# Kernel tuning notes

Hardware: AMD Instinct MI355X
Metric: run time of the kernel (lower is better)

The kernel has to match this reference:

```python
import jax, jax.numpy as jnp
import numpy as np

BN_EPS = 1e-5


def setup_inputs() -> dict:
    key = jax.random.key(0)
    ks = jax.random.split(key, 12)
    B, N, S, D1, D2 = 2, 16384, 4096, 128, 256
    C1, C2 = 256, 128  # mlp channels
    return {
        "xyz1": jax.random.normal(ks[0], (B, 3, N), dtype=jnp.float32),
        "xyz2": jax.random.normal(ks[1], (B, 3, S), dtype=jnp.float32),
        "points1": jax.random.normal(ks[2], (B, D1, N), dtype=jnp.float32),
        "points2": jax.random.normal(ks[3], (B, D2, S), dtype=jnp.float32),
        "w1": jax.random.normal(ks[4], (D1 + D2, C1), dtype=jnp.float32) * 0.05,
        "b1": jax.random.normal(ks[5], (C1,), dtype=jnp.float32) * 0.05,
        "g1": jax.random.uniform(ks[6], (C1,), dtype=jnp.float32, minval=0.5, maxval=1.5),
        "beta1": jax.random.normal(ks[7], (C1,), dtype=jnp.float32) * 0.05,
        "w2": jax.random.normal(ks[8], (C1, C2), dtype=jnp.float32) * 0.05,
        "b2": jax.random.normal(ks[9], (C2,), dtype=jnp.float32) * 0.05,
        "g2": jax.random.uniform(ks[10], (C2,), dtype=jnp.float32, minval=0.5, maxval=1.5),
        "beta2": jax.random.normal(ks[11], (C2,), dtype=jnp.float32) * 0.05,
    }


def _conv_bn_relu(x, W, b, g, beta):
    # 1x1 Conv1d == per-point matmul; BatchNorm1d training-mode stats over (B, N).
    y = x @ W + b                              # [B, N, Cout]
    mu = jnp.mean(y, axis=(0, 1))
    var = jnp.var(y, axis=(0, 1))              # biased variance, matches torch BN
    y = g * (y - mu) * jax.lax.rsqrt(var + BN_EPS) + beta
    return jax.nn.relu(y)


def reference(xyz1, xyz2, points1, points2, w1, b1, g1, beta1, w2, b2, g2, beta2):
    x1 = jnp.transpose(xyz1, (0, 2, 1))        # [B, N, 3]
    x2 = jnp.transpose(xyz2, (0, 2, 1))        # [B, S, 3]
    p2 = jnp.transpose(points2, (0, 2, 1))     # [B, S, D2]

    # squared pairwise distance [B, N, S], clamped at 0
    d = (jnp.sum(x1 ** 2, axis=-1, keepdims=True)
         - 2.0 * jnp.einsum('bnc,bsc->bns', x1, x2)
         + jnp.sum(x2 ** 2, axis=-1)[:, None, :])
    d = jnp.maximum(d, 0.0)

    # 3 nearest neighbors (ascending smallest distances) -- same math as full sort + slice
    neg_d3, idx = jax.lax.top_k(-d, 3)         # [B, N, 3]
    d3 = jnp.maximum(-neg_d3, 1e-6)
    recip = 1.0 / d3
    w = recip / jnp.maximum(jnp.sum(recip, axis=-1, keepdims=True), 1e-6)

    nb = jax.vmap(lambda p, i: p[i])(p2, idx)  # [B, N, 3, D2]
    interp = jnp.sum(nb * w[..., None], axis=2)
    interp = jnp.nan_to_num(interp, nan=0.0, posinf=0.0, neginf=0.0)

    p1 = jnp.transpose(points1, (0, 2, 1))     # [B, N, D1]
    x = jnp.concatenate([p1, interp], axis=-1) # [B, N, D1+D2]

    x = _conv_bn_relu(x, w1, b1, g1, beta1)
    x = _conv_bn_relu(x, w2, b2, g2, beta2)
    x = jnp.nan_to_num(x, nan=0.0, posinf=0.0, neginf=0.0)
    return jnp.transpose(x, (0, 2, 1))         # [B, C2, N]
```

## Files before the change

kernel.cpp:

```cpp
#include <hip/hip_runtime.h>

#define B_   2
#define N_   16384
#define S_   4096
#define D1_  128
#define D2_  256
#define C1_  256
#define C2_  128
#define M_   (B_ * N_)

typedef __bf16 bf16_t;
typedef bf16_t bf16x8 __attribute__((ext_vector_type(8)));
typedef float  f32x4  __attribute__((ext_vector_type(4)));

__device__ __forceinline__ void gload16(const void* g, void* l) {
  __builtin_amdgcn_global_load_lds(
      (const __attribute__((address_space(1))) void*)g,
      (__attribute__((address_space(3))) void*)l, 16, 0, 0);
}

__device__ __forceinline__ float med3a(float a, float b, float c) {
  float d;
  asm("v_med3_f32 %0, %1, %2, %3" : "=v"(d) : "v"(a), "v"(b), "v"(c));
  return d;
}

__device__ __forceinline__ float4 cand4(const float* __restrict__ X2, int i) {
  float x = X2[i], y = X2[S_ + i], z = X2[2 * S_ + i];
  float w = fmaf(x, x, fmaf(y, y, z * z));
  return make_float4(-2.f * x, -2.f * y, -2.f * z, w);
}
__device__ __forceinline__ float distv(float4 c, float ax, float ay, float az) {
  return fmaf(ax, c.x, fmaf(ay, c.y, fmaf(az, c.z, c.w)));
}
#define TRACK3(v)                                                        \
  {                                                                      \
    float t0_ = fminf((v), m0);                                          \
    float t1_ = med3a((v), m0, m1);                                      \
    float t2_ = med3a((v), m1, m2);                                      \
    m0 = t0_; m1 = t1_; m2 = t2_;                                        \
  }

union SMem1 {
  struct { float4 cbuf[1024]; float T3V[2][3][32]; float QMv[32][3]; } knn;
  float tile[2][32][33];
};

__global__ __launch_bounds__(512, 8) void phase1_k(const float* __restrict__ xyz1,
                                                   const float* __restrict__ xyz2,
                                                   const float* __restrict__ points1,
                                                   const float* __restrict__ w1,
                                                   const float* __restrict__ w2,
                                                   float* __restrict__ kw,
                                                   int* __restrict__ ki,
                                                   bf16_t* __restrict__ Xp1,
                                                   bf16_t* __restrict__ w1at,
                                                   bf16_t* __restrict__ w2t) {
  __shared__ SMem1 sm;
  int bi = blockIdx.x, t = threadIdx.x;
  if (bi < 1024) {
    int l = t & 63, w = t >> 6;
    int q = l & 31, h = l >> 5;
    int s = w * 2 + h;
    int b  = bi >> 9;
    int nb = (bi & 511) * 32;
    int n  = nb + q;
    const float* X1 = xyz1 + (size_t)b * 3 * N_;
    const float* X2 = xyz2 + (size_t)b * 3 * S_;
    float ax = X1[n], ay = X1[N_ + n], az = X1[2 * N_ + n];
    float p = fmaf(ax, ax, fmaf(ay, ay, az * az));
    float m0 = 3e38f, m1 = 3e38f, m2 = 3e38f;
    for (int r = 0; r < 4; ++r) {
      __syncthreads();
      sm.knn.cbuf[t]       = cand4(X2, r * 1024 + t);
      sm.knn.cbuf[t + 512] = cand4(X2, r * 1024 + t + 512);
      __syncthreads();
      const float4* cs = sm.knn.cbuf + s * 64;
#pragma unroll 16
      for (int i = 0; i < 64; ++i) {
        float v = distv(cs[i], ax, ay, az);
        TRACK3(v);
      }
    }
    __syncthreads();
    float* SV = (float*)sm.knn.cbuf;
    SV[(s * 3 + 0) * 32 + q] = m0;  SV[(s * 3 + 1) * 32 + q] = m1;  SV[(s * 3 + 2) * 32 + q] = m2;
    __syncthreads();
    if (t < 64) {
      int th = t >> 5, tq = t & 31;
      float m0 = 3e38f, m1 = 3e38f, m2 = 3e38f;
      for (int s2 = th * 8; s2 < th * 8 + 8; ++s2)
#pragma unroll
        for (int k = 0; k < 3; ++k) {
          float v = SV[(s2 * 3 + k) * 32 + tq];
          TRACK3(v);
        }
      sm.knn.T3V[th][0][tq] = m0; sm.knn.T3V[th][1][tq] = m1; sm.knn.T3V[th][2][tq] = m2;
    }
    __syncthreads();
    float g0 = 3e38f, g1 = 3e38f, g2 = 3e38f;
    if (t < 32) {
      float m0 = sm.knn.T3V[0][0][t], m1 = sm.knn.T3V[0][1][t], m2 = sm.knn.T3V[0][2][t];
#pragma unroll
      for (int k = 0; k < 3; ++k) {
        float v = sm.knn.T3V[1][k][t];
        TRACK3(v);
      }
      g0 = m0; g1 = m1; g2 = m2;
      sm.knn.QMv[t][0] = m0; sm.knn.QMv[t][1] = m1; sm.knn.QMv[t][2] = m2;
    }
    __syncthreads();
    float q0v = sm.knn.QMv[q][0], q1v = sm.knn.QMv[q][1], q2v = sm.knn.QMv[q][2];
    unsigned j0 = 0xFFFFFFFFu, j1 = 0xFFFFFFFFu, j2 = 0xFFFFFFFFu;
    for (int r = 0; r < 4; ++r) {
      __syncthreads();
      sm.knn.cbuf[t]       = cand4(X2, r * 1024 + t);
      sm.knn.cbuf[t + 512] = cand4(X2, r * 1024 + t + 512);
      __syncthreads();
      const float4* cs = sm.knn.cbuf + s * 64;
      int base = r * 1024 + s * 64;
#pragma unroll
      for (int g = 0; g < 16; ++g) {
        float v0 = distv(cs[g * 4 + 0], ax, ay, az);
        float v1 = distv(cs[g * 4 + 1], ax, ay, az);
        float v2 = distv(cs[g * 4 + 2], ax, ay, az);
        float v3 = distv(cs[g * 4 + 3], ax, ay, az);
        float gm = fminf(fminf(v0, v1), fminf(v2, v3));
        if (gm <= q2v) {
#define CHK(vv, uu)                                                      \
          {                                                              \
            unsigned idx = (unsigned)(base + g * 4 + uu);                \
            bool h0 = ((vv) == q0v) && (j0 == 0xFFFFFFFFu);              \
            bool h1 = ((vv) == q1v) && (j1 == 0xFFFFFFFFu) && !h0;       \
            bool h2 = ((vv) == q2v) && (j2 == 0xFFFFFFFFu) && !h0 && !h1;\
            if (h0) j0 = idx;                                            \
            if (h1) j1 = idx;                                            \
            if (h2) j2 = idx;                                            \
          }
          CHK(v0, 0) CHK(v1, 1) CHK(v2, 2) CHK(v3, 3)
#undef CHK
        }
      }
    }
    __syncthreads();
    unsigned* SI = (unsigned*)sm.knn.cbuf;
    SI[(s * 3 + 0) * 32 + q] = j0;  SI[(s * 3 + 1) * 32 + q] = j1;  SI[(s * 3 + 2) * 32 + q] = j2;
    __syncthreads();
    if (t < 32) {
      unsigned a0 = 0xFFFFFFFFu, a1 = 0xFFFFFFFFu, a2 = 0xFFFFFFFFu;
      for (int s2 = 0; s2 < 16; ++s2) {
        a0 = min(a0, SI[(s2 * 3 + 0) * 32 + t]);
        a1 = min(a1, SI[(s2 * 3 + 1) * 32 + t]);
        a2 = min(a2, SI[(s2 * 3 + 2) * 32 + t]);
      }
      a0 = min(a0, (unsigned)(S_ - 1));
      a1 = min(a1, (unsigned)(S_ - 1));
      a2 = min(a2, (unsigned)(S_ - 1));
      float d0 = fmaxf(p + g0, 1e-6f);
      float d1 = fmaxf(p + g1, 1e-6f);
      float d2 = fmaxf(p + g2, 1e-6f);
      float r0 = 1.f / d0, r1 = 1.f / d1, r2 = 1.f / d2;
      float dn = fmaxf(r0 + r1 + r2, 1e-6f);
      size_t rr = (size_t)b * N_ + n;
      kw[rr * 3 + 0] = r0 / dn;  kw[rr * 3 + 1] = r1 / dn;  kw[rr * 3 + 2] = r2 / dn;
      ki[rr * 3 + 0] = (int)a0;  ki[rr * 3 + 1] = (int)a1;  ki[rr * 3 + 2] = (int)a2;
    }
  } else if (bi < 3072) {
    int bj = bi - 1024;
    int b = bj >> 10, rest = bj & 1023;
    int n0 = (rest & 255) * 64, c0 = (rest >> 8) * 32;
    int tx = t & 31, ty = (t >> 5) & 7, th = t >> 8;
    const float* src = points1 + (size_t)b * D1_ * N_;
#pragma unroll
    for (int k = 0; k < 4; ++k)
      sm.tile[th][ty + k * 8][tx] = src[(size_t)(c0 + ty + k * 8) * N_ + n0 + th * 32 + tx];
    __syncthreads();
#pragma unroll
    for (int k = 0; k < 4; ++k)
      Xp1[(size_t)(b * N_ + n0 + th * 32 + ty + k * 8) * 128 + c0 + tx] =
          (bf16_t)sm.tile[th][tx][ty + k * 8];
  } else {
    int i = (bi - 3072) * 512 + t;
    if (i < 32768) {
      int n = i >> 7, k = i & 127;
      w1at[i] = (bf16_t)w1[(size_t)k * C1_ + n];
    } else {
      int j = i - 32768;
      int n = j >> 8, k = j & 255;
      w2t[j] = (bf16_t)w2[(size_t)k * C2_ + n];
    }
  }
}

__global__ __launch_bounds__(512) void gemmG_k(const float* __restrict__ points2,
                                               const float* __restrict__ w1,
                                               bf16_t* __restrict__ G) {
  const int LDP = 40;
  __shared__ bf16_t As[128 * LDP];
  __shared__ bf16_t Bs[256 * LDP];
  int t = threadIdx.x, lane = t & 63, w = t >> 6;
  int wr = w >> 2, wc = w & 3;
  int bb = blockIdx.x >> 5;
  int m0 = (blockIdx.x & 31) * 128;
  const float* P2 = points2 + (size_t)bb * D2_ * S_;
  f32x4 acc[4][4];
  f32x4 z = {0.f, 0.f, 0.f, 0.f};
#pragma unroll
  for (int i = 0; i < 4; ++i)
#pragma unroll
    for (int j = 0; j < 4; ++j) acc[i][j] = z;
  int sA = t & 127, kgA = t >> 7;
  int nB = t & 255, kgB = t >> 8;
  for (int k0 = 0; k0 < 256; k0 += 32) {
    __syncthreads();
    {
      bf16x8 ap;
#pragma unroll
      for (int kk = 0; kk < 8; ++kk)
        ap[kk] = (bf16_t)P2[(size_t)(k0 + kgA * 8 + kk) * S_ + m0 + sA];
      *(bf16x8*)&As[sA * LDP + kgA * 8] = ap;
      bf16x8 bp0, bp1;
#pragma unroll
      for (int kk = 0; kk < 8; ++kk) {
        bp0[kk] = (bf16_t)w1[(size_t)(128 + k0 + kgB * 16 + kk) * C1_ + nB];
        bp1[kk] = (bf16_t)w1[(size_t)(128 + k0 + kgB * 16 + 8 + kk) * C1_ + nB];
      }
      *(bf16x8*)&Bs[nB * LDP + kgB * 16] = bp0;
      *(bf16x8*)&Bs[nB * LDP + kgB * 16 + 8] = bp1;
    }
    __syncthreads();
    bf16x8 af[4], bfr[4];
    int arow = wr * 64 + (lane & 15);
    int brow = wc * 64 + (lane & 15);
    int kc = 8 * (lane >> 4);
#pragma unroll
    for (int i = 0; i < 4; ++i) af[i]  = *(const bf16x8*)&As[(arow + i * 16) * LDP + kc];
#pragma unroll
    for (int j = 0; j < 4; ++j) bfr[j] = *(const bf16x8*)&Bs[(brow + j * 16) * LDP + kc];
#pragma unroll
    for (int i = 0; i < 4; ++i)
#pragma unroll
      for (int j = 0; j < 4; ++j)
        acc[i][j] = __builtin_amdgcn_mfma_f32_16x16x32_bf16(af[i], bfr[j], acc[i][j], 0, 0, 0);
  }
  bf16_t* Gb = G + (size_t)bb * S_ * 256;
#pragma unroll
  for (int j = 0; j < 4; ++j) {
    int col = wc * 64 + j * 16 + (lane & 15);
#pragma unroll
    for (int i = 0; i < 4; ++i) {
      int r = m0 + wr * 64 + i * 16 + ((lane >> 4) << 2);
#pragma unroll
      for (int q = 0; q < 4; ++q)
        Gb[(size_t)(r + q) * 256 + col] = (bf16_t)acc[i][j][q];
    }
  }
}

__global__ __launch_bounds__(512) void gemm1_k(const bf16_t* __restrict__ A,
                                               const bf16_t* __restrict__ Bt,
                                               const float* __restrict__ bias,
                                               const bf16_t* __restrict__ G,
                                               const float* __restrict__ KW,
                                               const int* __restrict__ KI,
                                               bf16_t* __restrict__ Y,
                                               float* __restrict__ st) {
  const int K = 128;
  __shared__ bf16_t As[128 * 32];
  __shared__ bf16_t Bs[256 * 32];
  int tid = threadIdx.x, lane = tid & 63, w = tid >> 6;
  int wr = w >> 2, wc = w & 3;
  int m0 = blockIdx.x * 128;
  int ra = tid >> 2, ca = (tid & 3) * 8;
  f32x4 acc[4][4];
  f32x4 z = {0.f, 0.f, 0.f, 0.f};
#pragma unroll
  for (int i = 0; i < 4; ++i)
#pragma unroll
    for (int j = 0; j < 4; ++j) acc[i][j] = z;
  for (int k0 = 0; k0 < K; k0 += 32) {
    __syncthreads();
    gload16(A + (size_t)(m0 + ra) * K + k0 + ca, &As[ra * 32 + ca]);
    gload16(Bt + (size_t)ra * K + k0 + ca, &Bs[ra * 32 + ca]);
    gload16(Bt + (size_t)(128 + ra) * K + k0 + ca, &Bs[(128 + ra) * 32 + ca]);
    __syncthreads();
    bf16x8 af[4], bfr[4];
    int arow = wr * 64 + (lane & 15);
    int brow = wc * 64 + (lane & 15);
    int kc = 8 * (lane >> 4);
#pragma unroll
    for (int i = 0; i < 4; ++i) af[i]  = *(const bf16x8*)&As[(arow + i * 16) * 32 + kc];
#pragma unroll
    for (int j = 0; j < 4; ++j) bfr[j] = *(const bf16x8*)&Bs[(brow + j * 16) * 32 + kc];
#pragma unroll
    for (int i = 0; i < 4; ++i)
#pragma unroll
      for (int j = 0; j < 4; ++j)
        acc[i][j] = __builtin_amdgcn_mfma_f32_16x16x32_bf16(af[i], bfr[j], acc[i][j], 0, 0, 0);
  }
  __syncthreads();
  float* kwls = (float*)As;
  int*   kils = ((int*)As) + 384;
  if (tid < 128) {
    int r = m0 + tid;
    kwls[tid * 3 + 0] = KW[(size_t)r * 3 + 0];
    kwls[tid * 3 + 1] = KW[(size_t)r * 3 + 1];
    kwls[tid * 3 + 2] = KW[(size_t)r * 3 + 2];
    kils[tid * 3 + 0] = KI[(size_t)r * 3 + 0];
    kils[tid * 3 + 1] = KI[(size_t)r * 3 + 1];
    kils[tid * 3 + 2] = KI[(size_t)r * 3 + 2];
  }
  __syncthreads();
  int bb = m0 >> 14;
  const bf16_t* Gb = G + (size_t)bb * S_ * 256;
  float sjv[4]  = {0.f, 0.f, 0.f, 0.f};
  float ssjv[4] = {0.f, 0.f, 0.f, 0.f};
#pragma unroll
  for (int i = 0; i < 4; ++i) {
#pragma unroll
    for (int qq = 0; qq < 4; ++qq) {
      int rl = wr * 64 + i * 16 + ((lane >> 4) << 2) + qq;
      float w0 = kwls[rl * 3 + 0], w1v = kwls[rl * 3 + 1], w2v = kwls[rl * 3 + 2];
      const bf16_t* g0 = Gb + (size_t)kils[rl * 3 + 0] * 256;
      const bf16_t* g1 = Gb + (size_t)kils[rl * 3 + 1] * 256;
      const bf16_t* g2 = Gb + (size_t)kils[rl * 3 + 2] * 256;
      int r = m0 + rl;
#pragma unroll
      for (int j = 0; j < 4; ++j) {
        int col = wc * 64 + j * 16 + (lane & 15);
        float y = acc[i][j][qq] + bias[col]
                + w0 * (float)g0[col] + w1v * (float)g1[col] + w2v * (float)g2[col];
        Y[(size_t)r * C1_ + col] = (bf16_t)y;
        sjv[j] += y;  ssjv[j] += y * y;
      }
    }
  }
#pragma unroll
  for (int j = 0; j < 4; ++j) {
    float sj = sjv[j], ssj = ssjv[j];
    sj  += __shfl_xor(sj, 16);  sj  += __shfl_xor(sj, 32);
    ssj += __shfl_xor(ssj, 16); ssj += __shfl_xor(ssj, 32);
    if ((lane >> 4) == 0) {
      int col = wc * 64 + j * 16 + (lane & 15);
      atomicAdd(&st[col], sj);
      atomicAdd(&st[C1_ + col], ssj);
    }
  }
}

__global__ __launch_bounds__(256) void gemm2_k(const bf16_t* __restrict__ Y1,
                                               const bf16_t* __restrict__ Bt,
                                               const float* __restrict__ bias,
                                               const float* __restrict__ st1,
                                               const float* __restrict__ g1v,
                                               const float* __restrict__ be1,
                                               float* __restrict__ OUT,
                                               float* __restrict__ st2) {
  const int K = 256;
  __shared__ bf16_t As[128 * 32];
  __shared__ bf16_t Bs[128 * 32];
  __shared__ float sa1[C1_], sb1[C1_];
  int tid = threadIdx.x, lane = tid & 63, w = tid >> 6;
  int wr = w >> 1, wc = w & 1;
  int m0 = blockIdx.x * 128;
  {
    const float invM = 1.f / (float)M_;
    float mu  = st1[tid] * invM;
    float var = fmaxf(st1[C1_ + tid] * invM - mu * mu, 0.f);
    float a = g1v[tid] * rsqrtf(var + 1e-5f);
    sa1[tid] = a;
    sb1[tid] = be1[tid] - mu * a;
  }
  int e0 = (w * 2 + 0) * 512 + lane * 8;
  int e1 = (w * 2 + 1) * 512 + lane * 8;
  int ra0 = e0 >> 5, ca0 = e0 & 31;
  int ra1 = e1 >> 5, ca1 = e1 & 31;
  f32x4 acc[4][4];
  f32x4 z = {0.f, 0.f, 0.f, 0.f};
#pragma unroll
  for (int i = 0; i < 4; ++i)
#pragma unroll
    for (int j = 0; j < 4; ++j) acc[i][j] = z;
  bf16x8 va0 = *(const bf16x8*)&Y1[(size_t)(m0 + ra0) * C1_ + ca0];
  bf16x8 va1 = *(const bf16x8*)&Y1[(size_t)(m0 + ra1) * C1_ + ca1];
  __syncthreads();
  for (int k0 = 0; k0 < K; k0 += 32) {
    bf16x8 nb0, nb1;
    if (k0 + 32 < K) {
      nb0 = *(const bf16x8*)&Y1[(size_t)(m0 + ra0) * C1_ + k0 + 32 + ca0];
      nb1 = *(const bf16x8*)&Y1[(size_t)(m0 + ra1) * C1_ + k0 + 32 + ca1];
    }
    if (k0) __syncthreads();
    bf16x8 oa0, oa1;
#pragma unroll
    for (int u = 0; u < 8; ++u) {
      float f0 = (float)va0[u];
      float f1 = (float)va1[u];
      f0 = fmaxf(f0 * sa1[k0 + ca0 + u] + sb1[k0 + ca0 + u], 0.f);
      f1 = fmaxf(f1 * sa1[k0 + ca1 + u] + sb1[k0 + ca1 + u], 0.f);
      oa0[u] = (bf16_t)f0;
      oa1[u] = (bf16_t)f1;
    }
    *(bf16x8*)&As[e0] = oa0;
    *(bf16x8*)&As[e1] = oa1;
    gload16(Bt + (size_t)ra0 * K + k0 + ca0, &Bs[e0]);
    gload16(Bt + (size_t)ra1 * K + k0 + ca1, &Bs[e1]);
    __syncthreads();
    bf16x8 af[4], bfr[4];
    int arow = wr * 64 + (lane & 15);
    int brow = wc * 64 + (lane & 15);
    int kc = 8 * (lane >> 4);
#pragma unroll
    for (int i = 0; i < 4; ++i) af[i]  = *(const bf16x8*)&As[(arow + i * 16) * 32 + kc];
#pragma unroll
    for (int j = 0; j < 4; ++j) bfr[j] = *(const bf16x8*)&Bs[(brow + j * 16) * 32 + kc];
#pragma unroll
    for (int i = 0; i < 4; ++i)
#pragma unroll
      for (int j = 0; j < 4; ++j)
        acc[i][j] = __builtin_amdgcn_mfma_f32_16x16x32_bf16(af[i], bfr[j], acc[i][j], 0, 0, 0);
    va0 = nb0; va1 = nb1;
  }
#pragma unroll
  for (int j = 0; j < 4; ++j) {
    int col = wc * 64 + j * 16 + (lane & 15);
    float bv = bias[col];
    float sj = 0.f, ssj = 0.f;
#pragma unroll
    for (int i = 0; i < 4; ++i) {
      int r  = m0 + wr * 64 + i * 16 + ((lane >> 4) << 2);
      int bb = r >> 14, n = r & (N_ - 1);
      f32x4 v = acc[i][j];
#pragma unroll
      for (int q = 0; q < 4; ++q) {
        v[q] += bv;
        sj += v[q]; ssj += v[q] * v[q];
      }
      *(f32x4*)&OUT[((size_t)(bb * C2_ + col)) * N_ + n] = v;
    }
    sj  += __shfl_xor(sj, 16);  sj  += __shfl_xor(sj, 32);
    ssj += __shfl_xor(ssj, 16); ssj += __shfl_xor(ssj, 32);
    if ((lane >> 4) == 0) {
      atomicAdd(&st2[col], sj);
      atomicAdd(&st2[C2_ + col], ssj);
    }
  }
}

__global__ __launch_bounds__(256) void bn2apply_k(float* __restrict__ OUT,
                                                  const float* __restrict__ st,
                                                  const float* __restrict__ g,
                                                  const float* __restrict__ be) {
  __shared__ float ab[2];
  int t = threadIdx.x;
  int c = (blockIdx.x >> 4) & 127;
  if (t == 0) {
    const float invM = 1.f / (float)M_;
    float mu  = st[c] * invM;
    float var = fmaxf(st[C2_ + c] * invM - mu * mu, 0.f);
    float a = g[c] * rsqrtf(var + 1e-5f);
    ab[0] = a;
    ab[1] = be[c] - mu * a;
  }
  __syncthreads();
  float a = ab[0], s = ab[1];
  size_t i4 = (size_t)blockIdx.x * 256 + t;
  f32x4 v = *(f32x4*)&OUT[i4 * 4];
#pragma unroll
  for (int u = 0; u < 4; ++u) v[u] = fmaxf(a * v[u] + s, 0.f);
  *(f32x4*)&OUT[i4 * 4] = v;
}

extern "C" void kernel_launch(void* const* d_in, const int* in_sizes, int n_in,
                              void* d_out, int out_size, void* d_ws, size_t ws_size,
                              hipStream_t stream) {
  const float* xyz1    = (const float*)d_in[0];
  const float* xyz2    = (const float*)d_in[1];
  const float* points1 = (const float*)d_in[2];
  const float* points2 = (const float*)d_in[3];
  const float* w1      = (const float*)d_in[4];
  const float* b1      = (const float*)d_in[5];
  const float* g1      = (const float*)d_in[6];
  const float* beta1   = (const float*)d_in[7];
  const float* w2      = (const float*)d_in[8];
  const float* b2      = (const float*)d_in[9];
  const float* g2      = (const float*)d_in[10];
  const float* beta2   = (const float*)d_in[11];
  float* out = (float*)d_out;

  char* p = (char*)d_ws;
  size_t off = 0;
  bf16_t* Xp1  = (bf16_t*)(p + off); off += (size_t)M_ * 128 * 2;
  bf16_t* W1AT = (bf16_t*)(p + off); off += (size_t)C1_ * 128 * 2;
  bf16_t* W2T  = (bf16_t*)(p + off); off += (size_t)C2_ * C1_ * 2;
  bf16_t* G    = (bf16_t*)(p + off); off += (size_t)B_ * S_ * 256 * 2;
  bf16_t* Y1   = (bf16_t*)(p + off); off += (size_t)M_ * C1_ * 2;
  float*  KW   = (float*)(p + off);  off += (size_t)M_ * 3 * 4;
  int*    KI   = (int*)(p + off);    off += (size_t)M_ * 3 * 4;
  float*  ST1  = (float*)(p + off);  off += 2048;
  float*  ST2  = (float*)(p + off);  off += 1024;

  hipMemsetAsync(ST1, 0, 3072, stream);

  phase1_k<<<3200, 512, 0, stream>>>(xyz1, xyz2, points1, w1, w2,
                                     KW, KI, Xp1, W1AT, W2T);
  gemmG_k<<<64, 512, 0, stream>>>(points2, w1, G);
  gemm1_k<<<M_ / 128, 512, 0, stream>>>(Xp1, W1AT, b1, G, KW, KI, Y1, ST1);
  gemm2_k<<<M_ / 128, 256, 0, stream>>>(Y1, W2T, b2, ST1, g1, beta1, out, ST2);
  bn2apply_k<<<4096, 256, 0, stream>>>(out, ST2, g2, beta2);
}
```

Baseline: 130.0 us.

## Fold G GEMM into phase1 and fuse BN2 apply into gemm2 via grid barrier

The standalone points2×W1b GEMM moves into the phase1 launch as 128 extra blocks, each computing a 128×128 tile so it fits the shared-memory union. The stats zeroing moves into phase1, replacing the separate memset. The final BN2+ReLU pass becomes the tail of gemm2: a global atomic counter barrier waits for all blocks' statistics, then each block normalizes its own output tile. This removes two kernel launches and a memset, and reuses the output while it may still be cached. It relies on all 256 gemm2 blocks being co-resident; if they are not, the spin barrier deadlocks.

```diff
diff --git a/kernel.cpp b/kernel.cpp
--- a/kernel.cpp
+++ b/kernel.cpp
@@ -41,21 +41,27 @@
     m0 = t0_; m1 = t1_; m2 = t2_;                                        \
   }
 
+#define LDPG 40
+
 union SMem1 {
   struct { float4 cbuf[1024]; float T3V[2][3][32]; float QMv[32][3]; } knn;
+  struct { bf16_t As[128 * LDPG]; bf16_t Bs[128 * LDPG]; } gg;
   float tile[2][32][33];
 };
 
 __global__ __launch_bounds__(512, 8) void phase1_k(const float* __restrict__ xyz1,
                                                    const float* __restrict__ xyz2,
                                                    const float* __restrict__ points1,
+                                                   const float* __restrict__ points2,
                                                    const float* __restrict__ w1,
                                                    const float* __restrict__ w2,
                                                    float* __restrict__ kw,
                                                    int* __restrict__ ki,
                                                    bf16_t* __restrict__ Xp1,
                                                    bf16_t* __restrict__ w1at,
-                                                   bf16_t* __restrict__ w2t) {
+                                                   bf16_t* __restrict__ w2t,
+                                                   bf16_t* __restrict__ G,
+                                                   float* __restrict__ stz) {
   __shared__ SMem1 sm;
   int bi = blockIdx.x, t = threadIdx.x;
   if (bi < 1024) {
@@ -179,7 +185,10 @@
     for (int k = 0; k < 4; ++k)
       Xp1[(size_t)(b * N_ + n0 + th * 32 + ty + k * 8) * 128 + c0 + tx] =
           (bf16_t)sm.tile[th][tx][ty + k * 8];
-  } else {
+  } else if (bi < 3200) {
+    if (bi == 3072) {
+      for (int z = t; z < 772; z += 512) stz[z] = 0.f;
+    }
     int i = (bi - 3072) * 512 + t;
     if (i < 32768) {
       int n = i >> 7, k = i & 127;
@@ -189,70 +198,56 @@
       int n = j >> 8, k = j & 255;
       w2t[j] = (bf16_t)w2[(size_t)k * C2_ + n];
     }
-  }
-}
-
-__global__ __launch_bounds__(512) void gemmG_k(const float* __restrict__ points2,
-                                               const float* __restrict__ w1,
-                                               bf16_t* __restrict__ G) {
-  const int LDP = 40;
-  __shared__ bf16_t As[128 * LDP];
-  __shared__ bf16_t Bs[256 * LDP];
-  int t = threadIdx.x, lane = t & 63, w = t >> 6;
-  int wr = w >> 2, wc = w & 3;
-  int bb = blockIdx.x >> 5;
-  int m0 = (blockIdx.x & 31) * 128;
-  const float* P2 = points2 + (size_t)bb * D2_ * S_;
-  f32x4 acc[4][4];
-  f32x4 z = {0.f, 0.f, 0.f, 0.f};
-#pragma unroll
-  for (int i = 0; i < 4; ++i)
-#pragma unroll
-    for (int j = 0; j < 4; ++j) acc[i][j] = z;
-  int sA = t & 127, kgA = t >> 7;
-  int nB = t & 255, kgB = t >> 8;
-  for (int k0 = 0; k0 < 256; k0 += 32) {
-    __syncthreads();
-    {
-      bf16x8 ap;
-#pragma unroll
-      for (int kk = 0; kk < 8; ++kk)
-        ap[kk] = (bf16_t)P2[(size_t)(k0 + kgA * 8 + kk) * S_ + m0 + sA];
-      *(bf16x8*)&As[sA * LDP + kgA * 8] = ap;
-      bf16x8 bp0, bp1;
-#pragma unroll
-      for (int kk = 0; kk < 8; ++kk) {
-        bp0[kk] = (bf16_t)w1[(size_t)(128 + k0 + kgB * 16 + kk) * C1_ + nB];
-        bp1[kk] = (bf16_t)w1[(size_t)(128 + k0 + kgB * 16 + 8 + kk) * C1_ + nB];
-      }
-      *(bf16x8*)&Bs[nB * LDP + kgB * 16] = bp0;
-      *(bf16x8*)&Bs[nB * LDP + kgB * 16 + 8] = bp1;
-    }
-    __syncthreads();
-    bf16x8 af[4], bfr[4];
-    int arow = wr * 64 + (lane & 15);
-    int brow = wc * 64 + (lane & 15);
-    int kc = 8 * (lane >> 4);
-#pragma unroll
-    for (int i = 0; i < 4; ++i) af[i]  = *(const bf16x8*)&As[(arow + i * 16) * LDP + kc];
-#pragma unroll
-    for (int j = 0; j < 4; ++j) bfr[j] = *(const bf16x8*)&Bs[(brow + j * 16) * LDP + kc];
-#pragma unroll
-    for (int i = 0; i < 4; ++i)
-#pragma unroll
-      for (int j = 0; j < 4; ++j)
-        acc[i][j] = __builtin_amdgcn_mfma_f32_16x16x32_bf16(af[i], bfr[j], acc[i][j], 0, 0, 0);
-  }
-  bf16_t* Gb = G + (size_t)bb * S_ * 256;
-#pragma unroll
-  for (int j = 0; j < 4; ++j) {
-    int col = wc * 64 + j * 16 + (lane & 15);
-#pragma unroll
-    for (int i = 0; i < 4; ++i) {
-      int r = m0 + wr * 64 + i * 16 + ((lane >> 4) << 2);
-#pragma unroll
-      for (int q = 0; q < 4; ++q)
-        Gb[(size_t)(r + q) * 256 + col] = (bf16_t)acc[i][j][q];
+  } else {
+    int idx = bi - 3200;
+    int bb = idx >> 6, rem = idx & 63;
+    int m0 = (rem >> 1) * 128, n0 = (rem & 1) * 128;
+    const float* P2 = points2 + (size_t)bb * D2_ * S_;
+    int lane = t & 63, w = t >> 6;
+    int wr = w >> 2, wc = w & 3;
+    f32x4 acc[4][2];
+    f32x4 z = {0.f, 0.f, 0.f, 0.f};
+#pragma unroll
+    for (int i = 0; i < 4; ++i) { acc[i][0] = z; acc[i][1] = z; }
+    int sA = t & 127, kg = t >> 7;
+    for (int k0 = 0; k0 < 256; k0 += 32) {
+      __syncthreads();
+      {
+        bf16x8 ap, bp;
+#pragma unroll
+        for (int kk = 0; kk < 8; ++kk) {
+          ap[kk] = (bf16_t)P2[(size_t)(k0 + kg * 8 + kk) * S_ + m0 + sA];
+          bp[kk] = (bf16_t)w1[(size_t)(128 + k0 + kg * 8 + kk) * C1_ + n0 + sA];
+        }
+        *(bf16x8*)&sm.gg.As[sA * LDPG + kg * 8] = ap;
+        *(bf16x8*)&sm.gg.Bs[sA * LDPG + kg * 8] = bp;
+      }
+      __syncthreads();
+      int arow = wr * 64 + (lane & 15);
+      int brow = wc * 32 + (lane & 15);
+      int kc = 8 * (lane >> 4);
+      bf16x8 bfr[2];
+#pragma unroll
+      for (int j = 0; j < 2; ++j) bfr[j] = *(const bf16x8*)&sm.gg.Bs[(brow + j * 16) * LDPG + kc];
+#pragma unroll
+      for (int i = 0; i < 4; ++i) {
+        bf16x8 af = *(const bf16x8*)&sm.gg.As[(arow + i * 16) * LDPG + kc];
+#pragma unroll
+        for (int j = 0; j < 2; ++j)
+          acc[i][j] = __builtin_amdgcn_mfma_f32_16x16x32_bf16(af, bfr[j], acc[i][j], 0, 0, 0);
+      }
+    }
+    bf16_t* Gb = G + (size_t)bb * S_ * 256;
+#pragma unroll
+    for (int j = 0; j < 2; ++j) {
+      int col = n0 + wc * 32 + j * 16 + (lane & 15);
+#pragma unroll
+      for (int i = 0; i < 4; ++i) {
+        int r = m0 + wr * 64 + i * 16 + ((lane >> 4) << 2);
+#pragma unroll
+        for (int q = 0; q < 4; ++q)
+          Gb[(size_t)(r + q) * 256 + col] = (bf16_t)acc[i][j][q];
+      }
     }
   }
 }
@@ -355,7 +350,10 @@
                                                const float* __restrict__ g1v,
                                                const float* __restrict__ be1,
                                                float* __restrict__ OUT,
-                                               float* __restrict__ st2) {
+                                               float* __restrict__ st2,
+                                               const float* __restrict__ g2v,
+                                               const float* __restrict__ be2,
+                                               int* __restrict__ cnt) {
   const int K = 256;
   __shared__ bf16_t As[128 * 32];
   __shared__ bf16_t Bs[128 * 32];
@@ -445,30 +443,36 @@
       atomicAdd(&st2[C2_ + col], ssj);
     }
   }
-}
-
-__global__ __launch_bounds__(256) void bn2apply_k(float* __restrict__ OUT,
-                                                  const float* __restrict__ st,
-                                                  const float* __restrict__ g,
-                                                  const float* __restrict__ be) {
-  __shared__ float ab[2];
-  int t = threadIdx.x;
-  int c = (blockIdx.x >> 4) & 127;
-  if (t == 0) {
+  __syncthreads();
+  if (tid == 0) {
+    __threadfence();
+    atomicAdd(cnt, 1);
+    while (__hip_atomic_load(cnt, __ATOMIC_ACQUIRE, __HIP_MEMORY_SCOPE_AGENT) < (int)gridDim.x)
+      __builtin_amdgcn_s_sleep(8);
+  }
+  __syncthreads();
+  if (tid < C2_) {
+    float s  = __hip_atomic_load(&st2[tid],       __ATOMIC_RELAXED, __HIP_MEMORY_SCOPE_AGENT);
+    float ss = __hip_atomic_load(&st2[C2_ + tid], __ATOMIC_RELAXED, __HIP_MEMORY_SCOPE_AGENT);
     const float invM = 1.f / (float)M_;
-    float mu  = st[c] * invM;
-    float var = fmaxf(st[C2_ + c] * invM - mu * mu, 0.f);
-    float a = g[c] * rsqrtf(var + 1e-5f);
-    ab[0] = a;
-    ab[1] = be[c] - mu * a;
+    float mu  = s * invM;
+    float var = fmaxf(ss * invM - mu * mu, 0.f);
+    float a = g2v[tid] * rsqrtf(var + 1e-5f);
+    sa1[tid] = a;
+    sb1[tid] = be2[tid] - mu * a;
   }
   __syncthreads();
-  float a = ab[0], s = ab[1];
-  size_t i4 = (size_t)blockIdx.x * 256 + t;
-  f32x4 v = *(f32x4*)&OUT[i4 * 4];
-#pragma unroll
-  for (int u = 0; u < 4; ++u) v[u] = fmaxf(a * v[u] + s, 0.f);
-  *(f32x4*)&OUT[i4 * 4] = v;
+  int bb = m0 >> 14, ng = m0 & (N_ - 1);
+  int c = tid >> 1, half = tid & 1;
+  float a = sa1[c], sft = sb1[c];
+  float* pr = OUT + ((size_t)(bb * C2_ + c)) * N_ + ng + half * 64;
+#pragma unroll
+  for (int u2 = 0; u2 < 16; ++u2) {
+    f32x4 v = *(f32x4*)&pr[u2 * 4];
+#pragma unroll
+    for (int u = 0; u < 4; ++u) v[u] = fmaxf(a * v[u] + sft, 0.f);
+    *(f32x4*)&pr[u2 * 4] = v;
+  }
 }
 
 extern "C" void kernel_launch(void* const* d_in, const int* in_sizes, int n_in,
@@ -499,13 +503,12 @@
   int*    KI   = (int*)(p + off);    off += (size_t)M_ * 3 * 4;
   float*  ST1  = (float*)(p + off);  off += 2048;
   float*  ST2  = (float*)(p + off);  off += 1024;
-
-  hipMemsetAsync(ST1, 0, 3072, stream);
-
-  phase1_k<<<3200, 512, 0, stream>>>(xyz1, xyz2, points1, w1, w2,
-                                     KW, KI, Xp1, W1AT, W2T);
-  gemmG_k<<<64, 512, 0, stream>>>(points2, w1, G);
+  int*    CNT  = (int*)(p + off);    off += 16;
+
+
+  phase1_k<<<3328, 512, 0, stream>>>(xyz1, xyz2, points1, points2, w1, w2,
+                                     KW, KI, Xp1, W1AT, W2T, G, ST1);
   gemm1_k<<<M_ / 128, 512, 0, stream>>>(Xp1, W1AT, b1, G, KW, KI, Y1, ST1);
-  gemm2_k<<<M_ / 128, 256, 0, stream>>>(Y1, W2T, b2, ST1, g1, beta1, out, ST2);
-  bn2apply_k<<<4096, 256, 0, stream>>>(out, ST2, g2, beta2);
-}
+  gemm2_k<<<M_ / 128, 256, 0, stream>>>(Y1, W2T, b2, ST1, g1, beta1,
+                                        out, ST2, g2, beta2, CNT);
+}
```

Measured after the change: 138.3 us. 1.06x slower.

## Fuse both GEMMs and BN2 apply into one persistent kernel with grid barriers

Applied to the files above, without the earlier changes.

Merges gemm1, gemm2 and bn2apply into a single kernel launched with 256 blocks. Each block keeps its 128-row Y1 tile in LDS instead of writing it to global memory. Two atomic-counter grid barriers wait until the BN1 and BN2 statistics are complete, and then each block normalizes its own tile in place. The separate memset is dropped: the stats buffers and counters are zeroed inside phase1. This removes the Y1 global write and read and two kernel launches. In exchange it relies on every block being co-resident (about 94KB of LDS per block), runs at low occupancy, and pays for the spin-wait barriers.

```diff
diff --git a/kernel.cpp b/kernel.cpp
--- a/kernel.cpp
+++ b/kernel.cpp
@@ -55,7 +55,8 @@
                                                    int* __restrict__ ki,
                                                    bf16_t* __restrict__ Xp1,
                                                    bf16_t* __restrict__ w1at,
-                                                   bf16_t* __restrict__ w2t) {
+                                                   bf16_t* __restrict__ w2t,
+                                                   float* __restrict__ stz) {
   __shared__ SMem1 sm;
   int bi = blockIdx.x, t = threadIdx.x;
   if (bi < 1024) {
@@ -180,6 +181,9 @@
       Xp1[(size_t)(b * N_ + n0 + th * 32 + ty + k * 8) * 128 + c0 + tx] =
           (bf16_t)sm.tile[th][tx][ty + k * 8];
   } else {
+    if (bi == 3072) {
+      for (int z = t; z < 772; z += 512) stz[z] = 0.f;
+    }
     int i = (bi - 3072) * 512 + t;
     if (i < 32768) {
       int n = i >> 7, k = i & 127;
@@ -257,17 +261,28 @@
   }
 }
 
-__global__ __launch_bounds__(512) void gemm1_k(const bf16_t* __restrict__ A,
-                                               const bf16_t* __restrict__ Bt,
-                                               const float* __restrict__ bias,
-                                               const bf16_t* __restrict__ G,
-                                               const float* __restrict__ KW,
-                                               const int* __restrict__ KI,
-                                               bf16_t* __restrict__ Y,
-                                               float* __restrict__ st) {
-  const int K = 128;
+#define LDY 264
+
+__global__ __launch_bounds__(512) void gemm12_k(const bf16_t* __restrict__ A,
+                                                const bf16_t* __restrict__ W1t,
+                                                const float* __restrict__ b1v,
+                                                const bf16_t* __restrict__ G,
+                                                const float* __restrict__ KW,
+                                                const int* __restrict__ KI,
+                                                float* __restrict__ st1,
+                                                const float* __restrict__ g1v,
+                                                const float* __restrict__ be1,
+                                                const bf16_t* __restrict__ W2t,
+                                                const float* __restrict__ b2v,
+                                                float* __restrict__ OUT,
+                                                float* __restrict__ st2,
+                                                const float* __restrict__ g2v,
+                                                const float* __restrict__ be2,
+                                                int* __restrict__ cnt) {
   __shared__ bf16_t As[128 * 32];
   __shared__ bf16_t Bs[256 * 32];
+  __shared__ bf16_t Y1L[128 * LDY];
+  __shared__ float sc1[C1_], sc2[C1_];
   int tid = threadIdx.x, lane = tid & 63, w = tid >> 6;
   int wr = w >> 2, wc = w & 3;
   int m0 = blockIdx.x * 128;
@@ -278,11 +293,11 @@
   for (int i = 0; i < 4; ++i)
 #pragma unroll
     for (int j = 0; j < 4; ++j) acc[i][j] = z;
-  for (int k0 = 0; k0 < K; k0 += 32) {
-    __syncthreads();
-    gload16(A + (size_t)(m0 + ra) * K + k0 + ca, &As[ra * 32 + ca]);
-    gload16(Bt + (size_t)ra * K + k0 + ca, &Bs[ra * 32 + ca]);
-    gload16(Bt + (size_t)(128 + ra) * K + k0 + ca, &Bs[(128 + ra) * 32 + ca]);
+  for (int k0 = 0; k0 < 128; k0 += 32) {
+    __syncthreads();
+    gload16(A + (size_t)(m0 + ra) * 128 + k0 + ca, &As[ra * 32 + ca]);
+    gload16(W1t + (size_t)ra * 128 + k0 + ca, &Bs[ra * 32 + ca]);
+    gload16(W1t + (size_t)(128 + ra) * 128 + k0 + ca, &Bs[(128 + ra) * 32 + ca]);
     __syncthreads();
     bf16x8 af[4], bfr[4];
     int arow = wr * 64 + (lane & 15);
@@ -313,130 +328,111 @@
   __syncthreads();
   int bb = m0 >> 14;
   const bf16_t* Gb = G + (size_t)bb * S_ * 256;
-  float sjv[4]  = {0.f, 0.f, 0.f, 0.f};
-  float ssjv[4] = {0.f, 0.f, 0.f, 0.f};
-#pragma unroll
-  for (int i = 0; i < 4; ++i) {
-#pragma unroll
-    for (int qq = 0; qq < 4; ++qq) {
-      int rl = wr * 64 + i * 16 + ((lane >> 4) << 2) + qq;
-      float w0 = kwls[rl * 3 + 0], w1v = kwls[rl * 3 + 1], w2v = kwls[rl * 3 + 2];
-      const bf16_t* g0 = Gb + (size_t)kils[rl * 3 + 0] * 256;
-      const bf16_t* g1 = Gb + (size_t)kils[rl * 3 + 1] * 256;
-      const bf16_t* g2 = Gb + (size_t)kils[rl * 3 + 2] * 256;
-      int r = m0 + rl;
-#pragma unroll
-      for (int j = 0; j < 4; ++j) {
+  {
+    float sjv[4]  = {0.f, 0.f, 0.f, 0.f};
+    float ssjv[4] = {0.f, 0.f, 0.f, 0.f};
+#pragma unroll
+    for (int i = 0; i < 4; ++i) {
+#pragma unroll
+      for (int qq = 0; qq < 4; ++qq) {
+        int rl = wr * 64 + i * 16 + ((lane >> 4) << 2) + qq;
+        float w0 = kwls[rl * 3 + 0], w1v = kwls[rl * 3 + 1], w2v = kwls[rl * 3 + 2];
+        const bf16_t* g0 = Gb + (size_t)kils[rl * 3 + 0] * 256;
+        const bf16_t* g1 = Gb + (size_t)kils[rl * 3 + 1] * 256;
+        const bf16_t* g2 = Gb + (size_t)kils[rl * 3 + 2] * 256;
+#pragma unroll
+        for (int j = 0; j < 4; ++j) {
+          int col = wc * 64 + j * 16 + (lane & 15);
+          float y = acc[i][j][qq] + b1v[col]
+                  + w0 * (float)g0[col] + w1v * (float)g1[col] + w2v * (float)g2[col];
+          Y1L[rl * LDY + col] = (bf16_t)y;
+          sjv[j] += y;  ssjv[j] += y * y;
+        }
+      }
+    }
+#pragma unroll
+    for (int j = 0; j < 4; ++j) {
+      float sj = sjv[j], ssj = ssjv[j];
+      sj  += __shfl_xor(sj, 16);  sj  += __shfl_xor(sj, 32);
+      ssj += __shfl_xor(ssj, 16); ssj += __shfl_xor(ssj, 32);
+      if ((lane >> 4) == 0) {
         int col = wc * 64 + j * 16 + (lane & 15);
-        float y = acc[i][j][qq] + bias[col]
-                + w0 * (float)g0[col] + w1v * (float)g1[col] + w2v * (float)g2[col];
-        Y[(size_t)r * C1_ + col] = (bf16_t)y;
-        sjv[j] += y;  ssjv[j] += y * y;
-      }
-    }
-  }
-#pragma unroll
-  for (int j = 0; j < 4; ++j) {
-    float sj = sjv[j], ssj = ssjv[j];
-    sj  += __shfl_xor(sj, 16);  sj  += __shfl_xor(sj, 32);
-    ssj += __shfl_xor(ssj, 16); ssj += __shfl_xor(ssj, 32);
-    if ((lane >> 4) == 0) {
-      int col = wc * 64 + j * 16 + (lane & 15);
-      atomicAdd(&st[col], sj);
-      atomicAdd(&st[C1_ + col], ssj);
-    }
-  }
-}
-
-__global__ __launch_bounds__(256) void gemm2_k(const bf16_t* __restrict__ Y1,
-                                               const bf16_t* __restrict__ Bt,
-                                               const float* __restrict__ bias,
-                                               const float* __restrict__ st1,
-                                               const float* __restrict__ g1v,
-                                               const float* __restrict__ be1,
-                                               float* __restrict__ OUT,
-                                               float* __restrict__ st2) {
-  const int K = 256;
-  __shared__ bf16_t As[128 * 32];
-  __shared__ bf16_t Bs[128 * 32];
-  __shared__ float sa1[C1_], sb1[C1_];
-  int tid = threadIdx.x, lane = tid & 63, w = tid >> 6;
-  int wr = w >> 1, wc = w & 1;
-  int m0 = blockIdx.x * 128;
-  {
+        atomicAdd(&st1[col], sj);
+        atomicAdd(&st1[C1_ + col], ssj);
+      }
+    }
+  }
+  __syncthreads();
+  if (tid == 0) {
+    __threadfence();
+    atomicAdd(&cnt[0], 1);
+    while (__hip_atomic_load(&cnt[0], __ATOMIC_ACQUIRE, __HIP_MEMORY_SCOPE_AGENT) < (int)gridDim.x)
+      __builtin_amdgcn_s_sleep(8);
+  }
+  __syncthreads();
+  if (tid < C1_) {
+    float s  = __hip_atomic_load(&st1[tid],       __ATOMIC_RELAXED, __HIP_MEMORY_SCOPE_AGENT);
+    float ss = __hip_atomic_load(&st1[C1_ + tid], __ATOMIC_RELAXED, __HIP_MEMORY_SCOPE_AGENT);
     const float invM = 1.f / (float)M_;
-    float mu  = st1[tid] * invM;
-    float var = fmaxf(st1[C1_ + tid] * invM - mu * mu, 0.f);
+    float mu  = s * invM;
+    float var = fmaxf(ss * invM - mu * mu, 0.f);
     float a = g1v[tid] * rsqrtf(var + 1e-5f);
-    sa1[tid] = a;
-    sb1[tid] = be1[tid] - mu * a;
-  }
-  int e0 = (w * 2 + 0) * 512 + lane * 8;
-  int e1 = (w * 2 + 1) * 512 + lane * 8;
-  int ra0 = e0 >> 5, ca0 = e0 & 31;
-  int ra1 = e1 >> 5, ca1 = e1 & 31;
-  f32x4 acc[4][4];
-  f32x4 z = {0.f, 0.f, 0.f, 0.f};
-#pragma unroll
-  for (int i = 0; i < 4; ++i)
-#pragma unroll
-    for (int j = 0; j < 4; ++j) acc[i][j] = z;
-  bf16x8 va0 = *(const bf16x8*)&Y1[(size_t)(m0 + ra0) * C1_ + ca0];
-  bf16x8 va1 = *(const bf16x8*)&Y1[(size_t)(m0 + ra1) * C1_ + ca1];
-  __syncthreads();
-  for (int k0 = 0; k0 < K; k0 += 32) {
-    bf16x8 nb0, nb1;
-    if (k0 + 32 < K) {
-      nb0 = *(const bf16x8*)&Y1[(size_t)(m0 + ra0) * C1_ + k0 + 32 + ca0];
-      nb1 = *(const bf16x8*)&Y1[(size_t)(m0 + ra1) * C1_ + k0 + 32 + ca1];
-    }
-    if (k0) __syncthreads();
-    bf16x8 oa0, oa1;
-#pragma unroll
-    for (int u = 0; u < 8; ++u) {
-      float f0 = (float)va0[u];
-      float f1 = (float)va1[u];
-      f0 = fmaxf(f0 * sa1[k0 + ca0 + u] + sb1[k0 + ca0 + u], 0.f);
-      f1 = fmaxf(f1 * sa1[k0 + ca1 + u] + sb1[k0 + ca1 + u], 0.f);
-      oa0[u] = (bf16_t)f0;
-      oa1[u] = (bf16_t)f1;
-    }
-    *(bf16x8*)&As[e0] = oa0;
-    *(bf16x8*)&As[e1] = oa1;
-    gload16(Bt + (size_t)ra0 * K + k0 + ca0, &Bs[e0]);
-    gload16(Bt + (size_t)ra1 * K + k0 + ca1, &Bs[e1]);
-    __syncthreads();
-    bf16x8 af[4], bfr[4];
+    sc1[tid] = a;
+    sc2[tid] = be1[tid] - mu * a;
+  }
+  __syncthreads();
+#pragma unroll
+  for (int u = 0; u < 8; ++u) {
+    int chunk = tid * 8 + u;
+    int row = chunk >> 5, cc = (chunk & 31) * 8;
+    bf16x8 v = *(bf16x8*)&Y1L[row * LDY + cc];
+    bf16x8 o;
+#pragma unroll
+    for (int u2 = 0; u2 < 8; ++u2) {
+      float f = (float)v[u2];
+      f = fmaxf(f * sc1[cc + u2] + sc2[cc + u2], 0.f);
+      o[u2] = (bf16_t)f;
+    }
+    *(bf16x8*)&Y1L[row * LDY + cc] = o;
+  }
+  __syncthreads();
+  f32x4 acc2[4][2];
+#pragma unroll
+  for (int i = 0; i < 4; ++i) { acc2[i][0] = z; acc2[i][1] = z; }
+  for (int k0 = 0; k0 < 256; k0 += 32) {
+    __syncthreads();
+    gload16(W2t + (size_t)ra * 256 + k0 + ca, &Bs[ra * 32 + ca]);
+    __syncthreads();
+    bf16x8 af[4], bfr[2];
     int arow = wr * 64 + (lane & 15);
-    int brow = wc * 64 + (lane & 15);
+    int brow = wc * 32 + (lane & 15);
     int kc = 8 * (lane >> 4);
 #pragma unroll
-    for (int i = 0; i < 4; ++i) af[i]  = *(const bf16x8*)&As[(arow + i * 16) * 32 + kc];
-#pragma unroll
-    for (int j = 0; j < 4; ++j) bfr[j] = *(const bf16x8*)&Bs[(brow + j * 16) * 32 + kc];
+    for (int i = 0; i < 4; ++i) af[i]  = *(const bf16x8*)&Y1L[(arow + i * 16) * LDY + k0 + kc];
+#pragma unroll
+    for (int j = 0; j < 2; ++j) bfr[j] = *(const bf16x8*)&Bs[(brow + j * 16) * 32 + kc];
 #pragma unroll
     for (int i = 0; i < 4; ++i)
 #pragma unroll
-      for (int j = 0; j < 4; ++j)
-        acc[i][j] = __builtin_amdgcn_mfma_f32_16x16x32_bf16(af[i], bfr[j], acc[i][j], 0, 0, 0);
-    va0 = nb0; va1 = nb1;
-  }
-#pragma unroll
-  for (int j = 0; j < 4; ++j) {
-    int col = wc * 64 + j * 16 + (lane & 15);
-    float bv = bias[col];
+      for (int j = 0; j < 2; ++j)
+        acc2[i][j] = __builtin_amdgcn_mfma_f32_16x16x32_bf16(af[i], bfr[j], acc2[i][j], 0, 0, 0);
+  }
+  int ng = m0 & (N_ - 1);
+#pragma unroll
+  for (int j = 0; j < 2; ++j) {
+    int col = wc * 32 + j * 16 + (lane & 15);
+    float bv = b2v[col];
     float sj = 0.f, ssj = 0.f;
 #pragma unroll
     for (int i = 0; i < 4; ++i) {
-      int r  = m0 + wr * 64 + i * 16 + ((lane >> 4) << 2);
-      int bb = r >> 14, n = r & (N_ - 1);
-      f32x4 v = acc[i][j];
+      int rl = wr * 64 + i * 16 + ((lane >> 4) << 2);
+      f32x4 v = acc2[i][j];
 #pragma unroll
       for (int q = 0; q < 4; ++q) {
         v[q] += bv;
         sj += v[q]; ssj += v[q] * v[q];
       }
-      *(f32x4*)&OUT[((size_t)(bb * C2_ + col)) * N_ + n] = v;
+      *(f32x4*)&OUT[((size_t)(bb * C2_ + col)) * N_ + ng + rl] = v;
     }
     sj  += __shfl_xor(sj, 16);  sj  += __shfl_xor(sj, 32);
     ssj += __shfl_xor(ssj, 16); ssj += __shfl_xor(ssj, 32);
@@ -445,30 +441,37 @@
       atomicAdd(&st2[C2_ + col], ssj);
     }
   }
-}
-
-__global__ __launch_bounds__(256) void bn2apply_k(float* __restrict__ OUT,
-                                                  const float* __restrict__ st,
-                                                  const float* __restrict__ g,
-                                                  const float* __restrict__ be) {
-  __shared__ float ab[2];
-  int t = threadIdx.x;
-  int c = (blockIdx.x >> 4) & 127;
-  if (t == 0) {
+  __syncthreads();
+  if (tid == 0) {
+    __threadfence();
+    atomicAdd(&cnt[1], 1);
+    while (__hip_atomic_load(&cnt[1], __ATOMIC_ACQUIRE, __HIP_MEMORY_SCOPE_AGENT) < (int)gridDim.x)
+      __builtin_amdgcn_s_sleep(8);
+  }
+  __syncthreads();
+  if (tid < C2_) {
+    float s  = __hip_atomic_load(&st2[tid],       __ATOMIC_RELAXED, __HIP_MEMORY_SCOPE_AGENT);
+    float ss = __hip_atomic_load(&st2[C2_ + tid], __ATOMIC_RELAXED, __HIP_MEMORY_SCOPE_AGENT);
     const float invM = 1.f / (float)M_;
-    float mu  = st[c] * invM;
-    float var = fmaxf(st[C2_ + c] * invM - mu * mu, 0.f);
-    float a = g[c] * rsqrtf(var + 1e-5f);
-    ab[0] = a;
-    ab[1] = be[c] - mu * a;
-  }
-  __syncthreads();
-  float a = ab[0], s = ab[1];
-  size_t i4 = (size_t)blockIdx.x * 256 + t;
-  f32x4 v = *(f32x4*)&OUT[i4 * 4];
-#pragma unroll
-  for (int u = 0; u < 4; ++u) v[u] = fmaxf(a * v[u] + s, 0.f);
-  *(f32x4*)&OUT[i4 * 4] = v;
+    float mu  = s * invM;
+    float var = fmaxf(ss * invM - mu * mu, 0.f);
+    float a = g2v[tid] * rsqrtf(var + 1e-5f);
+    sc1[tid] = a;
+    sc2[tid] = be2[tid] - mu * a;
+  }
+  __syncthreads();
+  {
+    int c = tid >> 2, q4 = tid & 3;
+    float a = sc1[c], sft = sc2[c];
+    float* pr = OUT + ((size_t)(bb * C2_ + c)) * N_ + ng + q4 * 32;
+#pragma unroll
+    for (int u2 = 0; u2 < 8; ++u2) {
+      f32x4 v = *(f32x4*)&pr[u2 * 4];
+#pragma unroll
+      for (int u = 0; u < 4; ++u) v[u] = fmaxf(a * v[u] + sft, 0.f);
+      *(f32x4*)&pr[u2 * 4] = v;
+    }
+  }
 }
 
 extern "C" void kernel_launch(void* const* d_in, const int* in_sizes, int n_in,
@@ -494,18 +497,16 @@
   bf16_t* W1AT = (bf16_t*)(p + off); off += (size_t)C1_ * 128 * 2;
   bf16_t* W2T  = (bf16_t*)(p + off); off += (size_t)C2_ * C1_ * 2;
   bf16_t* G    = (bf16_t*)(p + off); off += (size_t)B_ * S_ * 256 * 2;
-  bf16_t* Y1   = (bf16_t*)(p + off); off += (size_t)M_ * C1_ * 2;
   float*  KW   = (float*)(p + off);  off += (size_t)M_ * 3 * 4;
   int*    KI   = (int*)(p + off);    off += (size_t)M_ * 3 * 4;
   float*  ST1  = (float*)(p + off);  off += 2048;
   float*  ST2  = (float*)(p + off);  off += 1024;
-
-  hipMemsetAsync(ST1, 0, 3072, stream);
+  int*    CNT  = (int*)(p + off);    off += 16;
+
 
   phase1_k<<<3200, 512, 0, stream>>>(xyz1, xyz2, points1, w1, w2,
-                                     KW, KI, Xp1, W1AT, W2T);
+                                     KW, KI, Xp1, W1AT, W2T, ST1);
   gemmG_k<<<64, 512, 0, stream>>>(points2, w1, G);
-  gemm1_k<<<M_ / 128, 512, 0, stream>>>(Xp1, W1AT, b1, G, KW, KI, Y1, ST1);
-  gemm2_k<<<M_ / 128, 256, 0, stream>>>(Y1, W2T, b2, ST1, g1, beta1, out, ST2);
-  bn2apply_k<<<4096, 256, 0, stream>>>(out, ST2, g2, beta2);
-}
+  gemm12_k<<<256, 512, 0, stream>>>(Xp1, W1AT, b1, G, KW, KI, ST1, g1, beta1,
+                                    W2T, b2, out, ST2, g2, beta2, CNT);
+}
```

Measured after the change: 148.1 us. +14.0%, slower.

## Fuse BN2 apply into gemm2 via grid barrier and drop stats memset

Applied to the files above, without the earlier changes.

Zeroing of the BN stat accumulators and the barrier counter moves into one phase1 block, which removes the separate memset. The standalone bn2apply kernel is folded into gemm2. Each block signals completion through an atomic counter and spins until all 256 blocks have arrived, then computes the BN2 scale and shift and normalises its own just-written output tile in place. This saves a kernel launch and a separate full pass over the output, and the re-read may hit in cache. In exchange it relies on all gemm2 blocks being co-resident, otherwise the spin-wait deadlocks, and it adds barrier spin time.

```diff
diff --git a/kernel.cpp b/kernel.cpp
--- a/kernel.cpp
+++ b/kernel.cpp
@@ -55,7 +55,8 @@
                                                    int* __restrict__ ki,
                                                    bf16_t* __restrict__ Xp1,
                                                    bf16_t* __restrict__ w1at,
-                                                   bf16_t* __restrict__ w2t) {
+                                                   bf16_t* __restrict__ w2t,
+                                                   float* __restrict__ stz) {
   __shared__ SMem1 sm;
   int bi = blockIdx.x, t = threadIdx.x;
   if (bi < 1024) {
@@ -180,6 +181,9 @@
       Xp1[(size_t)(b * N_ + n0 + th * 32 + ty + k * 8) * 128 + c0 + tx] =
           (bf16_t)sm.tile[th][tx][ty + k * 8];
   } else {
+    if (bi == 3072) {
+      for (int z = t; z < 772; z += 512) stz[z] = 0.f;
+    }
     int i = (bi - 3072) * 512 + t;
     if (i < 32768) {
       int n = i >> 7, k = i & 127;
@@ -355,7 +359,10 @@
                                                const float* __restrict__ g1v,
                                                const float* __restrict__ be1,
                                                float* __restrict__ OUT,
-                                               float* __restrict__ st2) {
+                                               float* __restrict__ st2,
+                                               const float* __restrict__ g2v,
+                                               const float* __restrict__ be2,
+                                               int* __restrict__ cnt) {
   const int K = 256;
   __shared__ bf16_t As[128 * 32];
   __shared__ bf16_t Bs[128 * 32];
@@ -445,30 +452,36 @@
       atomicAdd(&st2[C2_ + col], ssj);
     }
   }
-}
-
-__global__ __launch_bounds__(256) void bn2apply_k(float* __restrict__ OUT,
-                                                  const float* __restrict__ st,
-                                                  const float* __restrict__ g,
-                                                  const float* __restrict__ be) {
-  __shared__ float ab[2];
-  int t = threadIdx.x;
-  int c = (blockIdx.x >> 4) & 127;
-  if (t == 0) {
+  __syncthreads();
+  if (tid == 0) {
+    __threadfence();
+    atomicAdd(cnt, 1);
+    while (__hip_atomic_load(cnt, __ATOMIC_ACQUIRE, __HIP_MEMORY_SCOPE_AGENT) < (int)gridDim.x)
+      __builtin_amdgcn_s_sleep(8);
+  }
+  __syncthreads();
+  if (tid < C2_) {
+    float s  = __hip_atomic_load(&st2[tid],       __ATOMIC_RELAXED, __HIP_MEMORY_SCOPE_AGENT);
+    float ss = __hip_atomic_load(&st2[C2_ + tid], __ATOMIC_RELAXED, __HIP_MEMORY_SCOPE_AGENT);
     const float invM = 1.f / (float)M_;
-    float mu  = st[c] * invM;
-    float var = fmaxf(st[C2_ + c] * invM - mu * mu, 0.f);
-    float a = g[c] * rsqrtf(var + 1e-5f);
-    ab[0] = a;
-    ab[1] = be[c] - mu * a;
+    float mu  = s * invM;
+    float var = fmaxf(ss * invM - mu * mu, 0.f);
+    float a = g2v[tid] * rsqrtf(var + 1e-5f);
+    sa1[tid] = a;
+    sb1[tid] = be2[tid] - mu * a;
   }
   __syncthreads();
-  float a = ab[0], s = ab[1];
-  size_t i4 = (size_t)blockIdx.x * 256 + t;
-  f32x4 v = *(f32x4*)&OUT[i4 * 4];
-#pragma unroll
-  for (int u = 0; u < 4; ++u) v[u] = fmaxf(a * v[u] + s, 0.f);
-  *(f32x4*)&OUT[i4 * 4] = v;
+  int bb = m0 >> 14, ng = m0 & (N_ - 1);
+  int c = tid >> 1, half = tid & 1;
+  float a = sa1[c], sft = sb1[c];
+  float* pr = OUT + ((size_t)(bb * C2_ + c)) * N_ + ng + half * 64;
+#pragma unroll
+  for (int u2 = 0; u2 < 16; ++u2) {
+    f32x4 v = *(f32x4*)&pr[u2 * 4];
+#pragma unroll
+    for (int u = 0; u < 4; ++u) v[u] = fmaxf(a * v[u] + sft, 0.f);
+    *(f32x4*)&pr[u2 * 4] = v;
+  }
 }
 
 extern "C" void kernel_launch(void* const* d_in, const int* in_sizes, int n_in,
@@ -499,13 +512,13 @@
   int*    KI   = (int*)(p + off);    off += (size_t)M_ * 3 * 4;
   float*  ST1  = (float*)(p + off);  off += 2048;
   float*  ST2  = (float*)(p + off);  off += 1024;
-
-  hipMemsetAsync(ST1, 0, 3072, stream);
+  int*    CNT  = (int*)(p + off);    off += 16;
+
 
   phase1_k<<<3200, 512, 0, stream>>>(xyz1, xyz2, points1, w1, w2,
-                                     KW, KI, Xp1, W1AT, W2T);
+                                     KW, KI, Xp1, W1AT, W2T, ST1);
   gemmG_k<<<64, 512, 0, stream>>>(points2, w1, G);
   gemm1_k<<<M_ / 128, 512, 0, stream>>>(Xp1, W1AT, b1, G, KW, KI, Y1, ST1);
-  gemm2_k<<<M_ / 128, 256, 0, stream>>>(Y1, W2T, b2, ST1, g1, beta1, out, ST2);
-  bn2apply_k<<<4096, 256, 0, stream>>>(out, ST2, g2, beta2);
-}
+  gemm2_k<<<M_ / 128, 256, 0, stream>>>(Y1, W2T, b2, ST1, g1, beta1,
+                                        out, ST2, g2, beta2, CNT);
+}
```

After: 151.0 us. 1.16x slower.
